# Performance work log

Measured on AMD Instinct MI355X. Metric: run time of the kernel, lower is better.

Reference implementation:

```python
import jax, jax.numpy as jnp
import numpy as np
import math

GAMMA = 2.0
ALPHA = 0.25
SIZES = [[64, 64], [32, 32], [16, 16], [8, 8], [4, 4]]
RATIOS = [0.5, 1.0, 2.0]
SCALES = [1.0, 2.0 ** (1.0 / 3.0), 2.0 ** (2.0 / 3.0)]
B, T, C = 16, 64, 80


def _create_anchors(sizes, ratios, scales):
    # replicates torch create_anchors (cthw format, normalized [-1,1] coords)
    aspects = np.array([[[s * math.sqrt(r), s * math.sqrt(1.0 / r)] for s in scales]
                        for r in ratios], dtype=np.float64).reshape(-1, 2)
    out = []
    for (h, w) in sizes:
        sized = 4.0 * (aspects * np.array([2.0 / h, 2.0 / w]))  # [a,2]
        rows = np.linspace(-1 + 1.0 / h, 1 - 1.0 / h, h) if h > 1 else np.array([0.0])
        cols = np.linspace(-1 + 1.0 / w, 1 - 1.0 / w, w) if w > 1 else np.array([0.0])
        gy, gx = np.meshgrid(rows, cols, indexing='ij')
        grid = np.stack([gy, gx], -1).reshape(-1, 1, 2)  # [h*w,1,2]
        n, a = grid.shape[0], aspects.shape[0]
        anc = np.concatenate([np.broadcast_to(grid, (n, a, 2)),
                              np.broadcast_to(sized[None], (n, a, 2))], 2)
        out.append(anc.reshape(-1, 4))
    return jnp.asarray(np.concatenate(out, 0), dtype=jnp.float32)


def _cthw2tlbr(b):
    return jnp.concatenate([b[..., :2] - b[..., 2:] / 2, b[..., :2] + b[..., 2:] / 2], -1)


def _tlbr2cthw(b):
    return jnp.concatenate([(b[..., :2] + b[..., 2:]) / 2, b[..., 2:] - b[..., :2]], -1)


def _iou(anchors, tgts):
    # anchors [A,4] cthw, tgts [T,4] cthw -> [A,T]
    a_t, t_t = _cthw2tlbr(anchors), _cthw2tlbr(tgts)
    tl = jnp.maximum(a_t[:, None, :2], t_t[None, :, :2])
    br = jnp.minimum(a_t[:, None, 2:], t_t[None, :, 2:])
    sz = jnp.clip(br - tl, 0.0)
    inter = sz[..., 0] * sz[..., 1]
    a_sz = anchors[:, 2] * anchors[:, 3]
    t_sz = tgts[:, 2] * tgts[:, 3]
    union = a_sz[:, None] + t_sz[None, :] - inter
    return inter / (union + 1e-8)


def _bbox_to_activ(bboxes, anchors):
    tc = (bboxes[..., :2] - anchors[..., :2]) / anchors[..., 2:]
    ts = jnp.log(bboxes[..., 2:] / anchors[..., 2:] + 1e-8)
    return jnp.concatenate([tc, ts], -1) / jnp.array([0.1, 0.1, 0.2, 0.2], dtype=bboxes.dtype)


def _one_loss(clas_pred, bbox_pred, clas_tgt, bbox_tgt_tlbr, anchors):
    Tn = clas_tgt.shape[0]
    tgt = _tlbr2cthw(bbox_tgt_tlbr)
    valid = clas_tgt > 0                       # pad_idx = 0 -> padded targets invalid
    iou = jnp.where(valid[None, :], _iou(anchors, tgt), -1.0)  # [A,T]
    vals = iou.max(axis=1)
    idxs = iou.argmax(axis=1)
    # -1 background, -2 ignore band (0.4 <= iou <= 0.5)
    matches = jnp.where(vals > 0.5, idxs, jnp.where(vals < 0.4, -1, -2))
    pos = matches >= 0
    safe = jnp.clip(matches, 0, Tn - 1)
    # smooth_l1 (beta=1, mean over selected elements)
    reg_tgt = _bbox_to_activ(tgt[safe], anchors)
    d = bbox_pred - reg_tgt
    ad = jnp.abs(d)
    sl1 = jnp.where(ad < 1.0, 0.5 * d * d, ad - 0.5)
    npos = pos.sum().astype(clas_pred.dtype)
    bb_loss = (sl1 * pos[:, None]).sum() / jnp.maximum(4.0 * npos, 1.0)
    # class targets: matched anchors get 1-based class, background -> 0
    cls = jnp.where(pos, clas_tgt[safe], 0)
    clas_mask = matches >= -1                  # exclude ignored anchors
    enc = jax.nn.one_hot(cls - 1, clas_pred.shape[1], dtype=clas_pred.dtype)  # cls=0 -> all-zero row
    ps = jax.nn.sigmoid(clas_pred)
    w = (enc * (1 - ps) + (1 - enc) * ps) ** GAMMA * ((1 - enc) * ALPHA + enc * (1 - ALPHA))
    w = jax.lax.stop_gradient(w)               # weights.detach() in torch
    bce = -(enc * jax.nn.log_sigmoid(clas_pred) + (1 - enc) * jax.nn.log_sigmoid(-clas_pred))
    clas_loss = (w * bce * clas_mask[:, None].astype(clas_pred.dtype)).sum()
    return bb_loss + clas_loss / jnp.maximum(npos, 1.0)


def setup_inputs() -> dict:
    key = jax.random.key(0)
    k1, k2, k3, k4, k5 = jax.random.split(key, 5)
    anchors = _create_anchors(SIZES, RATIOS, SCALES)
    A = anchors.shape[0]
    clas_preds = jax.random.normal(k1, (B, A, C), dtype=jnp.float32)
    bbox_preds = jax.random.normal(k2, (B, A, 4), dtype=jnp.float32) * 0.1
    centers = jax.random.uniform(k3, (B, T, 2), minval=-0.7, maxval=0.7)
    sizes = jax.random.uniform(k4, (B, T, 2), minval=0.05, maxval=0.5)
    bbox_tgts = jnp.concatenate([centers - sizes / 2, centers + sizes / 2], -1)  # tlbr
    clas_tgts = jax.random.randint(k5, (B, T), 1, C + 1)  # 1-based labels, no padding
    return {"clas_preds": clas_preds, "bbox_preds": bbox_preds,
            "bbox_tgts": bbox_tgts, "clas_tgts": clas_tgts, "anchors": anchors}


def reference(clas_preds, bbox_preds, bbox_tgts, clas_tgts, anchors):
    per_img = jax.vmap(_one_loss, in_axes=(0, 0, 0, 0, None))(
        clas_preds, bbox_preds, clas_tgts, bbox_tgts, anchors)
    return per_img.sum() / clas_preds.shape[0]
```

## Files before the change

kernel.cpp:

```cpp
#include <hip/hip_runtime.h>
#include <cstdint>
#include <cstddef>

#define TPB 256
#define MAXT 128

#define K_BG 0.17328679514f

__device__ __forceinline__ float f_bg4(float4 v) {
    float r = 0.f;
    const float xs[4] = {v.x, v.y, v.z, v.w};
    #pragma unroll
    for (int i = 0; i < 4; ++i) {
        const float x  = xs[i];
        const float u  = x * 1.44269504089f;
        const float em = __builtin_amdgcn_exp2f(-fabsf(u));
        const float oe = 1.f + em;
        const float l2 = __builtin_amdgcn_logf(oe);
        const float s  = __builtin_amdgcn_rcpf(oe);
        const float sp2 = fmaxf(u, 0.f) + l2;
        const float p  = (x >= 0.f) ? s : (1.f - s);
        r = fmaf(p * p, sp2, r);
    }
    return r;
}

__device__ __forceinline__ float f_fg_minus_bg(float x) {
    const float ax = fabsf(x);
    const float em = __builtin_amdgcn_exp2f(ax * -1.44269504089f);
    const float oe = 1.f + em;
    const float l  = __builtin_amdgcn_logf(oe) * 0.69314718056f;
    const float s  = __builtin_amdgcn_rcpf(oe);
    const float sp_p = (x >= 0.f) ? (x + l) : l;
    const float sp_n = sp_p - x;
    const float p  = (x >= 0.f) ? s : (1.f - s);
    const float q  = 1.f - p;
    return 0.75f * q * q * sp_n - 0.25f * p * p * sp_p;
}

template<int C4T>
__global__ __launch_bounds__(TPB, 4)
void fused_kernel(const float* __restrict__ bbox_preds,
                  const float* __restrict__ bbox_tgts,
                  const int*   __restrict__ clas_tgts,
                  const float* __restrict__ anchors,
                  const float* __restrict__ clas_preds,
                  int A, int T, int C4rt,
                  float* __restrict__ np_p,
                  float* __restrict__ bb_p,
                  float* __restrict__ cl_p,
                  int nblk)
{
    const int C4  = (C4T > 0) ? C4T : C4rt;
    const int b   = blockIdx.y;
    const int a0  = blockIdx.x * TPB;
    const int tid = threadIdx.x;
    const int a   = a0 + tid;
    const bool in = (a < A);

    __shared__ float t_tl0[MAXT], t_tl1[MAXT], t_br0[MAXT], t_br1[MAXT];
    __shared__ float t_area[MAXT];
    __shared__ float t_c0[MAXT], t_c1[MAXT], t_s0[MAXT], t_s1[MAXT];
    __shared__ int   t_cls[MAXT];
    for (int i = tid; i < T; i += TPB) {
        const float4 tg = reinterpret_cast<const float4*>(bbox_tgts)[(size_t)b * T + i];
        const float c0 = (tg.x + tg.z) * 0.5f, c1 = (tg.y + tg.w) * 0.5f;
        const float s0 = tg.z - tg.x,          s1 = tg.w - tg.y;
        t_c0[i] = c0; t_c1[i] = c1; t_s0[i] = s0; t_s1[i] = s1;
        t_tl0[i] = c0 - s0 * 0.5f; t_tl1[i] = c1 - s1 * 0.5f;
        t_br0[i] = c0 + s0 * 0.5f; t_br1[i] = c1 + s1 * 0.5f;
        t_area[i] = s0 * s1;
        t_cls[i]  = clas_tgts[(size_t)b * T + i];
    }

    float4 anc = make_float4(0.f, 0.f, 1.f, 1.f);
    if (in) anc = reinterpret_cast<const float4*>(anchors)[a];

    const int nA = min(TPB, A - a0);
    const float4* tile = reinterpret_cast<const float4*>(clas_preds)
                         + ((size_t)b * A + a0) * C4;
    float raw = 0.f;
    if (C4T > 0 && nA == TPB) {
        constexpr int CH  = 4;
        constexpr int NCH = (C4T > 0 ? C4T : 4) / CH;
        float4 cur[CH], nxt[CH];
        #pragma unroll
        for (int i = 0; i < CH; ++i) cur[i] = tile[tid + i * TPB];
        #pragma unroll
        for (int g = 0; g < NCH; ++g) {
            if (g + 1 < NCH) {
                #pragma unroll
                for (int i = 0; i < CH; ++i)
                    nxt[i] = tile[tid + ((g + 1) * CH + i) * TPB];
            }
            #pragma unroll
            for (int i = 0; i < CH; ++i) raw += f_bg4(cur[i]);
            #pragma unroll
            for (int i = 0; i < CH; ++i) cur[i] = nxt[i];
        }
    } else {
        const int tot = nA * C4;
        for (int j = tid; j < tot; j += TPB)
            raw += f_bg4(tile[j]);
    }

    __syncthreads();

    const float a_tl0 = anc.x - anc.z * 0.5f;
    const float a_tl1 = anc.y - anc.w * 0.5f;
    const float a_br0 = anc.x + anc.z * 0.5f;
    const float a_br1 = anc.y + anc.w * 0.5f;
    const float a_area = anc.z * anc.w;

    float best = -1e30f;
    int   besti = 0;
    #pragma unroll 4
    for (int t = 0; t < T; ++t) {
        float iou = -1.0f;
        if (t_cls[t] > 0) {
            const float tl0 = fmaxf(a_tl0, t_tl0[t]);
            const float tl1 = fmaxf(a_tl1, t_tl1[t]);
            const float br0 = fminf(a_br0, t_br0[t]);
            const float br1 = fminf(a_br1, t_br1[t]);
            const float sz0 = fmaxf(br0 - tl0, 0.0f);
            const float sz1 = fmaxf(br1 - tl1, 0.0f);
            const float inter = sz0 * sz1;
            const float uni = a_area + t_area[t] - inter;
            iou = inter * __builtin_amdgcn_rcpf(uni + 1e-8f);
        }
        if (iou > best) { best = iou; besti = t; }
    }

    const bool pos = in && (best > 0.5f);
    const bool ign = in && !pos && !(best < 0.4f);

    float sl1 = 0.f;
    int   cls = 0;
    if (pos) {
        cls = t_cls[besti];
        const float4 bp = reinterpret_cast<const float4*>(bbox_preds)[(size_t)b * A + a];
        const float tc0 = (t_c0[besti] - anc.x) / anc.z;
        const float tc1 = (t_c1[besti] - anc.y) / anc.w;
        const float ts0 = logf(t_s0[besti] / anc.z + 1e-8f);
        const float ts1 = logf(t_s1[besti] / anc.w + 1e-8f);
        const float r0 = tc0 / 0.1f, r1 = tc1 / 0.1f;
        const float r2 = ts0 / 0.2f, r3 = ts1 / 0.2f;
        const float d0 = bp.x - r0, d1 = bp.y - r1, d2 = bp.z - r2, d3 = bp.w - r3;
        const float a0f = fabsf(d0), a1f = fabsf(d1), a2f = fabsf(d2), a3f = fabsf(d3);
        sl1 += (a0f < 1.f) ? 0.5f * d0 * d0 : a0f - 0.5f;
        sl1 += (a1f < 1.f) ? 0.5f * d1 * d1 : a1f - 0.5f;
        sl1 += (a2f < 1.f) ? 0.5f * d2 * d2 : a2f - 0.5f;
        sl1 += (a3f < 1.f) ? 0.5f * d3 * d3 : a3f - 0.5f;
    }

    const int lane = tid & 63;
    const int wid  = tid >> 6;
    const unsigned long long pball = __ballot(pos);
    const unsigned long long iball = __ballot(ign);

    __shared__ int s_pc[TPB / 64], s_ic[TPB / 64];
    __shared__ int s_plist[TPB], s_pcls[TPB], s_ilist[TPB];
    if (lane == 0) { s_pc[wid] = __popcll(pball); s_ic[wid] = __popcll(iball); }
    __syncthreads();
    int p_off = 0, i_off = 0, p_total = 0, i_total = 0;
    #pragma unroll
    for (int w = 0; w < TPB / 64; ++w) {
        if (w < wid) { p_off += s_pc[w]; i_off += s_ic[w]; }
        p_total += s_pc[w]; i_total += s_ic[w];
    }
    const unsigned long long lmask = (lane == 63) ? ~0ULL >> 1 : (1ULL << lane) - 1;
    if (pos) {
        const int idx = p_off + __popcll(pball & lmask);
        s_plist[idx] = a; s_pcls[idx] = cls;
    }
    if (ign) {
        const int idx = i_off + __popcll(iball & lmask);
        s_ilist[idx] = a;
    }
    __syncthreads();

    float corr = 0.f;
    if (tid < p_total) {
        const int pa = s_plist[tid];
        const int pc = s_pcls[tid];
        const float x = clas_preds[((size_t)b * A + pa) * (C4 * 4) + (pc - 1)];
        corr += f_fg_minus_bg(x);
    }
    const int ig_elems = i_total * C4;
    for (int j = tid; j < ig_elems; j += TPB) {
        const int ii = j / C4;
        const int c4 = j - ii * C4;
        const int ia = s_ilist[ii];
        raw -= f_bg4(reinterpret_cast<const float4*>(clas_preds)
                         [((size_t)b * A + ia) * C4 + c4]);
    }

    float v = sl1;
    float u = fmaf(raw, K_BG, corr);
    #pragma unroll
    for (int off = 32; off; off >>= 1) {
        v += __shfl_down(v, off);
        u += __shfl_down(u, off);
    }
    __shared__ float s_sl1[TPB / 64], s_cl[TPB / 64];
    if (lane == 0) { s_sl1[wid] = v; s_cl[wid] = u; }
    __syncthreads();
    if (tid == 0) {
        float tv = 0.f, tu = 0.f;
        #pragma unroll
        for (int w = 0; w < TPB / 64; ++w) { tv += s_sl1[w]; tu += s_cl[w]; }
        const size_t o = (size_t)b * nblk + blockIdx.x;
        bb_p[o] = tv;
        cl_p[o] = tu;
        np_p[o] = (float)p_total;
    }
}

__global__ void reduce_kernel(const float* __restrict__ np_p,
                              const float* __restrict__ bb_p,
                              const float* __restrict__ cl_p,
                              int nblk, int Bn,
                              float* __restrict__ out)
{
    const int wid  = threadIdx.x >> 6;
    const int lane = threadIdx.x & 63;
    const int nw   = blockDim.x >> 6;
    __shared__ float s_loss[32];

    float acc = 0.f;
    for (int b = wid; b < Bn; b += nw) {
        float cl = 0.f, bb = 0.f, np = 0.f;
        for (int i = lane; i < nblk; i += 64) {
            const size_t o = (size_t)b * nblk + i;
            np += np_p[o]; bb += bb_p[o]; cl += cl_p[o];
        }
        #pragma unroll
        for (int off = 32; off; off >>= 1) {
            cl += __shfl_down(cl, off);
            bb += __shfl_down(bb, off);
            np += __shfl_down(np, off);
        }
        if (lane == 0)
            acc += bb / fmaxf(4.f * np, 1.f) + cl / fmaxf(np, 1.f);
    }
    if (lane == 0) s_loss[wid] = acc;
    __syncthreads();
    if (threadIdx.x == 0) {
        float v = 0.f;
        for (int w = 0; w < nw; ++w) v += s_loss[w];
        out[0] = v / (float)Bn;
    }
}

extern "C" void kernel_launch(void* const* d_in, const int* in_sizes, int n_in,
                              void* d_out, int out_size, void* d_ws, size_t ws_size,
                              hipStream_t stream)
{
    const float* clas_preds = (const float*)d_in[0];
    const float* bbox_preds = (const float*)d_in[1];
    const float* bbox_tgts  = (const float*)d_in[2];
    const int*   clas_tgts  = (const int*)d_in[3];
    const float* anchors    = (const float*)d_in[4];

    const int A  = in_sizes[4] / 4;
    const int Bn = in_sizes[1] / (A * 4);
    const int T  = in_sizes[3] / Bn;
    const int C  = in_sizes[0] / (Bn * A);
    const int C4 = C / 4;

    const int nblk = (A + TPB - 1) / TPB;

    char* ws = (char*)d_ws;
    float* np_p = (float*)ws;  ws += (size_t)Bn * nblk * sizeof(float);
    float* bb_p = (float*)ws;  ws += (size_t)Bn * nblk * sizeof(float);
    float* cl_p = (float*)ws;

    dim3 g1((unsigned)nblk, (unsigned)Bn);
    if (C4 == 20) {
        fused_kernel<20><<<g1, TPB, 0, stream>>>(
            bbox_preds, bbox_tgts, clas_tgts, anchors, clas_preds,
            A, T, C4, np_p, bb_p, cl_p, nblk);
    } else {
        fused_kernel<0><<<g1, TPB, 0, stream>>>(
            bbox_preds, bbox_tgts, clas_tgts, anchors, clas_preds,
            A, T, C4, np_p, bb_p, cl_p, nblk);
    }

    reduce_kernel<<<1, 1024, 0, stream>>>(np_p, bb_p, cl_p, nblk, Bn, (float*)d_out);
}
```

Baseline: 76.02 us.

## Interleave IoU matching with class-pred streaming and pack target data into vector LDS

Moves the barrier before the class-prediction load loop and splits the per-anchor IoU loop over targets into chunks that run between prefetch groups. The long-latency global loads of clas_preds can then overlap with ALU work on the IoU scan. Target data is packed into float4/float2 shared arrays, and invalid targets get a sentinel box, so the per-target branch disappears and LDS reads are vectorised. The prefetch chunk size changes from 4 to 5 float4s, which raises register pressure. Targets with a negative IoU-sentinel path now give iou=0 rather than -1, which changes tie behaviour slightly.

```diff
diff --git a/kernel.cpp b/kernel.cpp
--- a/kernel.cpp
+++ b/kernel.cpp
@@ -58,36 +58,66 @@
     const int a   = a0 + tid;
     const bool in = (a < A);
 
-    __shared__ float t_tl0[MAXT], t_tl1[MAXT], t_br0[MAXT], t_br1[MAXT];
-    __shared__ float t_area[MAXT];
-    __shared__ float t_c0[MAXT], t_c1[MAXT], t_s0[MAXT], t_s1[MAXT];
-    __shared__ int   t_cls[MAXT];
+    __shared__ float4 s_ta[MAXT];
+    __shared__ float4 s_tb[MAXT];
+    __shared__ float2 s_tc[MAXT];
     for (int i = tid; i < T; i += TPB) {
         const float4 tg = reinterpret_cast<const float4*>(bbox_tgts)[(size_t)b * T + i];
+        const int   cl = clas_tgts[(size_t)b * T + i];
         const float c0 = (tg.x + tg.z) * 0.5f, c1 = (tg.y + tg.w) * 0.5f;
         const float s0 = tg.z - tg.x,          s1 = tg.w - tg.y;
-        t_c0[i] = c0; t_c1[i] = c1; t_s0[i] = s0; t_s1[i] = s1;
-        t_tl0[i] = c0 - s0 * 0.5f; t_tl1[i] = c1 - s1 * 0.5f;
-        t_br0[i] = c0 + s0 * 0.5f; t_br1[i] = c1 + s1 * 0.5f;
-        t_area[i] = s0 * s1;
-        t_cls[i]  = clas_tgts[(size_t)b * T + i];
+        const bool  val = (cl > 0);
+        s_ta[i] = val ? make_float4(c0 - s0 * 0.5f, c1 - s1 * 0.5f,
+                                    c0 + s0 * 0.5f, c1 + s1 * 0.5f)
+                      : make_float4(1e30f, 1e30f, -1e30f, -1e30f);
+        s_tb[i] = make_float4(c0, c1, s0, s1);
+        s_tc[i] = make_float2(val ? s0 * s1 : 0.f, (float)cl);
     }
 
     float4 anc = make_float4(0.f, 0.f, 1.f, 1.f);
     if (in) anc = reinterpret_cast<const float4*>(anchors)[a];
+    const float a_tl0 = anc.x - anc.z * 0.5f;
+    const float a_tl1 = anc.y - anc.w * 0.5f;
+    const float a_br0 = anc.x + anc.z * 0.5f;
+    const float a_br1 = anc.y + anc.w * 0.5f;
+    const float a_area = anc.z * anc.w;
+
+    __syncthreads();
 
     const int nA = min(TPB, A - a0);
     const float4* tile = reinterpret_cast<const float4*>(clas_preds)
                          + ((size_t)b * A + a0) * C4;
-    float raw = 0.f;
+
+    float raw  = 0.f;
+    float best = -1e30f;
+    int   besti = 0;
+
+#define IOU_STEP(t)                                                         \
+    {                                                                       \
+        const float4 ta = s_ta[t];                                          \
+        const float2 tc = s_tc[t];                                          \
+        const float tl0 = fmaxf(a_tl0, ta.x);                               \
+        const float tl1 = fmaxf(a_tl1, ta.y);                               \
+        const float br0 = fminf(a_br0, ta.z);                               \
+        const float br1 = fminf(a_br1, ta.w);                               \
+        const float sz0 = fmaxf(br0 - tl0, 0.0f);                           \
+        const float sz1 = fmaxf(br1 - tl1, 0.0f);                           \
+        const float inter = sz0 * sz1;                                      \
+        const float uni = a_area + tc.x - inter;                            \
+        const float iou = inter * __builtin_amdgcn_rcpf(uni + 1e-8f);       \
+        if (iou > best) { best = iou; besti = (t); }                        \
+    }
+
     if (C4T > 0 && nA == TPB) {
-        constexpr int CH  = 4;
-        constexpr int NCH = (C4T > 0 ? C4T : 4) / CH;
-        float4 cur[CH], nxt[CH];
+        constexpr int CH  = 5;
+        constexpr int NCH = (C4T > 0 ? C4T : 5) / CH;
+        const int TCH = T / NCH;
+        float4 cur[CH];
         #pragma unroll
         for (int i = 0; i < CH; ++i) cur[i] = tile[tid + i * TPB];
         #pragma unroll
         for (int g = 0; g < NCH; ++g) {
+            float4 nxt[CH];
             if (g + 1 < NCH) {
                 #pragma unroll
                 for (int i = 0; i < CH; ++i)
@@ -95,41 +125,23 @@
             }
             #pragma unroll
             for (int i = 0; i < CH; ++i) raw += f_bg4(cur[i]);
-            #pragma unroll
-            for (int i = 0; i < CH; ++i) cur[i] = nxt[i];
+            const int t0 = g * TCH;
+            #pragma unroll 4
+            for (int t = t0; t < t0 + TCH; ++t) IOU_STEP(t)
+            if (g + 1 < NCH) {
+                #pragma unroll
+                for (int i = 0; i < CH; ++i) cur[i] = nxt[i];
+            }
         }
+        for (int t = (T / NCH) * NCH; t < T; ++t) IOU_STEP(t)
     } else {
         const int tot = nA * C4;
         for (int j = tid; j < tot; j += TPB)
             raw += f_bg4(tile[j]);
-    }
-
-    __syncthreads();
-
-    const float a_tl0 = anc.x - anc.z * 0.5f;
-    const float a_tl1 = anc.y - anc.w * 0.5f;
-    const float a_br0 = anc.x + anc.z * 0.5f;
-    const float a_br1 = anc.y + anc.w * 0.5f;
-    const float a_area = anc.z * anc.w;
-
-    float best = -1e30f;
-    int   besti = 0;
-    #pragma unroll 4
-    for (int t = 0; t < T; ++t) {
-        float iou = -1.0f;
-        if (t_cls[t] > 0) {
-            const float tl0 = fmaxf(a_tl0, t_tl0[t]);
-            const float tl1 = fmaxf(a_tl1, t_tl1[t]);
-            const float br0 = fminf(a_br0, t_br0[t]);
-            const float br1 = fminf(a_br1, t_br1[t]);
-            const float sz0 = fmaxf(br0 - tl0, 0.0f);
-            const float sz1 = fmaxf(br1 - tl1, 0.0f);
-            const float inter = sz0 * sz1;
-            const float uni = a_area + t_area[t] - inter;
-            iou = inter * __builtin_amdgcn_rcpf(uni + 1e-8f);
-        }
-        if (iou > best) { best = iou; besti = t; }
-    }
+        #pragma unroll 4
+        for (int t = 0; t < T; ++t) IOU_STEP(t)
+    }
+#undef IOU_STEP
 
     const bool pos = in && (best > 0.5f);
     const bool ign = in && !pos && !(best < 0.4f);
@@ -137,12 +149,13 @@
     float sl1 = 0.f;
     int   cls = 0;
     if (pos) {
-        cls = t_cls[besti];
+        const float4 tb  = s_tb[besti];
+        cls = (int)s_tc[besti].y;
         const float4 bp = reinterpret_cast<const float4*>(bbox_preds)[(size_t)b * A + a];
-        const float tc0 = (t_c0[besti] - anc.x) / anc.z;
-        const float tc1 = (t_c1[besti] - anc.y) / anc.w;
-        const float ts0 = logf(t_s0[besti] / anc.z + 1e-8f);
-        const float ts1 = logf(t_s1[besti] / anc.w + 1e-8f);
+        const float tc0 = (tb.x - anc.x) / anc.z;
+        const float tc1 = (tb.y - anc.y) / anc.w;
+        const float ts0 = logf(tb.z / anc.z + 1e-8f);
+        const float ts1 = logf(tb.w / anc.w + 1e-8f);
         const float r0 = tc0 / 0.1f, r1 = tc1 / 0.1f;
         const float r2 = ts0 / 0.2f, r3 = ts1 / 0.2f;
         const float d0 = bp.x - r0, d1 = bp.y - r1, d2 = bp.z - r2, d3 = bp.w - r3;
```

Measured after the change: 65.23 us. 1.17x faster.
